# Kernel tuning notes

Measured on AMD Instinct MI355X. Metric: run time of the kernel, lower is better.

Reference implementation:

```python
import jax, jax.numpy as jnp
import numpy as np

N = 50000      # nodes
E = 800000     # edges (avg degree 16)
G = 256        # graphs in batch
IN = 128       # in_channels
H = 256        # hidden_channels
L = 4          # num_layers


def setup_inputs() -> dict:
    key = jax.random.key(0)
    ks = jax.random.split(key, 16)
    x = jax.random.normal(ks[0], (N, IN), dtype=jnp.float32)
    edge_index = jax.random.randint(ks[1], (2, E), 0, N, dtype=jnp.int64)
    batch = jnp.sort(jax.random.randint(ks[2], (N,), 0, G, dtype=jnp.int64))
    s_in = 1.0 / np.sqrt(IN)
    s_h = 1.0 / np.sqrt(H)
    return {
        "x": x,
        "edge_index": edge_index,
        "batch": batch,
        "w1_0": jax.random.normal(ks[3], (IN, H), jnp.float32) * s_in,
        "b1_0": jnp.zeros((H,), jnp.float32),
        "w2_0": jax.random.normal(ks[4], (H, H), jnp.float32) * s_h,
        "b2_0": jnp.zeros((H,), jnp.float32),
        "w1s": jax.random.normal(ks[5], (L - 1, H, H), jnp.float32) * s_h,
        "b1s": jnp.zeros((L - 1, H), jnp.float32),
        "w2s": jax.random.normal(ks[6], (L - 1, H, H), jnp.float32) * s_h,
        "b2s": jnp.zeros((L - 1, H), jnp.float32),
    }


def reference(x, edge_index, batch, w1_0, b1_0, w2_0, b2_0, w1s, b1s, w2s, b2s):
    n_nodes = x.shape[0]
    src, dst = edge_index[0], edge_index[1]

    def gin_layer(h, w1, b1, w2, b2):
        # scatter-add neighbor aggregation: out[i] = sum_{(j->i)} h[j]
        agg = jax.ops.segment_sum(h[src], dst, num_segments=n_nodes)
        z = h + agg  # GIN with eps = 0: (1+eps)*x + aggr
        z = jax.nn.relu(z @ w1 + b1) @ w2 + b2  # MLP: Linear-ReLU-Linear
        return jax.nn.relu(z)  # outer F.relu in forward

    h = gin_layer(x, w1_0, b1_0, w2_0, b2_0)
    for i in range(L - 1):  # small fixed layer loop
        h = gin_layer(h, w1s[i], b1s[i], w2s[i], b2s[i])

    # global_add_pool: per-graph segment sum -> [G, H]
    return jax.ops.segment_sum(h, batch, num_segments=G)
```

## Files before the change

kernel.cpp:

```cpp
#include <hip/hip_runtime.h>
#include <hip/hip_bf16.h>

#define NN 50000
#define NE 800000
#define NG 256
#define CIN 128
#define CH 256

typedef unsigned short u16;
typedef unsigned int u32;
typedef __attribute__((ext_vector_type(8))) short short8;
typedef __attribute__((ext_vector_type(8))) unsigned short ushort8;
typedef __attribute__((ext_vector_type(4))) float f32x4;

__device__ __forceinline__ float bf2f(u16 u) { return __uint_as_float(((u32)u) << 16); }
__device__ __forceinline__ u16 f2bf(float f) {
    u32 u = __float_as_uint(f);
    return (u16)((u + 0x7fffu + ((u >> 16) & 1u)) >> 16);
}

__global__ void k_prep(const float* __restrict__ x, u16* __restrict__ xb,
                       const float* __restrict__ w1_0, const float* __restrict__ w2_0,
                       const float* __restrict__ w1s, const float* __restrict__ w2s,
                       u16* __restrict__ Wp, int* __restrict__ deg_fill,
                       int* __restrict__ gs, int* __restrict__ ge,
                       float* __restrict__ outf) {
    int t = blockIdx.x * 256 + threadIdx.x;
    if (t < 2 * NN) deg_fill[t] = 0;
    if (t < NG) { gs[t] = 0; ge[t] = 0; }
    if (t < NG * CH) outf[t] = 0.f;
    if (t < NN * CIN / 4) {
        float4 v = ((const float4*)x)[t];
        ushort4 o; o.x = f2bf(v.x); o.y = f2bf(v.y); o.z = f2bf(v.z); o.w = f2bf(v.w);
        ((ushort4*)xb)[t] = o;
    }
    if (t < CIN * CH + 7 * CH * CH) {
        const float* Wsrc; int rem;
        if (t < CIN * CH) { Wsrc = w1_0; rem = t; }
        else {
            int o = t - CIN * CH;
            int m = o >> 16; rem = o & 65535;
            Wsrc = (m == 0) ? w2_0
                 : (m <= 3) ? w1s + (size_t)(m - 1) * 65536
                            : w2s + (size_t)(m - 4) * 65536;
        }
        int j = rem & 7, lane = (rem >> 3) & 63, nt = (rem >> 9) & 15, kb = rem >> 13;
        int k = kb * 32 + ((lane >> 4) << 3) + j;
        int nc = nt * 16 + (lane & 15);
        Wp[t] = f2bf(Wsrc[k * CH + nc]);
    }
}

__global__ void k_count_deg_bounds(const int* __restrict__ dst, int* __restrict__ deg,
                                   const int* __restrict__ batch,
                                   int* __restrict__ gs, int* __restrict__ ge) {
    int e = blockIdx.x * 256 + threadIdx.x;
    if (e < NE) atomicAdd(&deg[dst[e]], 1);
    if (e < NN) {
        int b = batch[e];
        if (e == 0 || batch[e - 1] != b) gs[b] = e;
        if (e == NN - 1 || batch[e + 1] != b) ge[b] = e + 1;
    }
}

__global__ void k_scan1(const int* __restrict__ deg, int* __restrict__ bsum) {
    __shared__ int sd[256];
    int base = blockIdx.x * 1024, t = threadIdx.x, s = 0;
    for (int j = 0; j < 4; j++) { int i = base + t * 4 + j; if (i < NN) s += deg[i]; }
    sd[t] = s; __syncthreads();
    for (int off = 128; off > 0; off >>= 1) { if (t < off) sd[t] += sd[t + off]; __syncthreads(); }
    if (t == 0) bsum[blockIdx.x] = sd[0];
}

__global__ void k_scan2(int* bsum, int nb, int* row_ptr) {
    int lane = threadIdx.x;
    int v = (lane < nb) ? bsum[lane] : 0;
    int s = v;
    for (int off = 1; off < 64; off <<= 1) {
        int t = __shfl_up(s, off, 64);
        if (lane >= off) s += t;
    }
    if (lane < nb) bsum[lane] = s - v;
    if (lane == 0) row_ptr[NN] = NE;
}

__global__ void k_scan3(const int* __restrict__ deg, const int* __restrict__ bsum,
                        int* __restrict__ row_ptr) {
    __shared__ int sd[256];
    int base = blockIdx.x * 1024, t = threadIdx.x;
    int v[4]; int s = 0;
    for (int j = 0; j < 4; j++) { int i = base + t * 4 + j; v[j] = (i < NN) ? deg[i] : 0; s += v[j]; }
    sd[t] = s; __syncthreads();
    for (int off = 1; off < 256; off <<= 1) {
        int tmp = (t >= off) ? sd[t - off] : 0; __syncthreads();
        sd[t] += tmp; __syncthreads();
    }
    int run = bsum[blockIdx.x] + sd[t] - s;
    for (int j = 0; j < 4; j++) { int i = base + t * 4 + j; if (i < NN) row_ptr[i] = run; run += v[j]; }
}

__global__ void k_fill(const int* __restrict__ src, const int* __restrict__ dst,
                       const int* __restrict__ row_ptr, int* __restrict__ fill,
                       int* __restrict__ col) {
    int e = blockIdx.x * 256 + threadIdx.x;
    if (e < NE) {
        int d = dst[e];
        int pos = row_ptr[d] + atomicAdd(&fill[d], 1);
        col[pos] = src[e];
    }
}

#define ZS 264
template <int K1>
__global__ __launch_bounds__(256, 8) void k_layer(const u16* __restrict__ G,
                                                  const int* __restrict__ row_ptr,
                                                  const int* __restrict__ col,
                                                  const u16* __restrict__ Wp1,
                                                  const float* __restrict__ b1,
                                                  const u16* __restrict__ Wp2,
                                                  const float* __restrict__ b2,
                                                  u16* __restrict__ out) {
    __shared__ __align__(16) u16 zs[32 * ZS];
    const int tid = threadIdx.x;
    const int wave = tid >> 6, lane = tid & 63;
    const int quad = lane >> 4, l16 = lane & 15;
    const int m0 = blockIdx.x * 32;

    constexpr int LPR = K1 / 8;
    constexpr int RPG = 64 / LPR;
    const int sub = lane / LPR;
    const int c0 = (lane % LPR) * 8;
    for (int g = 0; g < 8; g += RPG) {
        int lr = wave * 8 + g + sub;
        int r = m0 + lr; if (r >= NN) r = NN - 1;
        const u16* base = G + c0;
        float a[8];
        ushort8 sv = *(const ushort8*)(base + (size_t)r * K1);
#pragma unroll
        for (int i = 0; i < 8; i++) a[i] = bf2f(sv[i]);
        int beg = row_ptr[r], end = row_ptr[r + 1];
        int e = beg;
        for (; e + 4 <= end; e += 4) {
            ushort8 v0 = *(const ushort8*)(base + (size_t)col[e] * K1);
            ushort8 v1 = *(const ushort8*)(base + (size_t)col[e + 1] * K1);
            ushort8 v2 = *(const ushort8*)(base + (size_t)col[e + 2] * K1);
            ushort8 v3 = *(const ushort8*)(base + (size_t)col[e + 3] * K1);
#pragma unroll
            for (int i = 0; i < 8; i++)
                a[i] += bf2f(v0[i]) + bf2f(v1[i]) + bf2f(v2[i]) + bf2f(v3[i]);
        }
        for (; e < end; e++) {
            ushort8 nv = *(const ushort8*)(base + (size_t)col[e] * K1);
#pragma unroll
            for (int i = 0; i < 8; i++) a[i] += bf2f(nv[i]);
        }
        ushort8 o;
#pragma unroll
        for (int i = 0; i < 8; i++) o[i] = f2bf(a[i]);
        *(ushort8*)(zs + lr * ZS + c0) = o;
    }
    __syncthreads();

    f32x4 acc[2][4];
#pragma unroll
    for (int ri = 0; ri < 2; ri++)
#pragma unroll
        for (int nj = 0; nj < 4; nj++) acc[ri][nj] = (f32x4){0.f, 0.f, 0.f, 0.f};

    const u16* w1b = Wp1 + (wave * 4) * 512 + lane * 8;
    const u16* w2b = Wp2 + (wave * 4) * 512 + lane * 8;
    constexpr int KB1 = K1 / 32;
    short8 b_cur[4], b_nxt[4];
#pragma unroll
    for (int nj = 0; nj < 4; nj++) b_cur[nj] = *(const short8*)(w1b + nj * 512);

#pragma unroll
    for (int kb = 0; kb < KB1; kb++) {
        int kn = (kb + 1 < KB1) ? (kb + 1) : kb;
#pragma unroll
        for (int nj = 0; nj < 4; nj++)
            b_nxt[nj] = *(const short8*)(w1b + kn * 8192 + nj * 512);
        short8 a[2];
#pragma unroll
        for (int ri = 0; ri < 2; ri++)
            a[ri] = *(const short8*)(zs + (ri * 16 + l16) * ZS + kb * 32 + quad * 8);
#pragma unroll
        for (int nj = 0; nj < 4; nj++)
#pragma unroll
            for (int ri = 0; ri < 2; ri++)
                acc[ri][nj] = __builtin_amdgcn_mfma_f32_16x16x32_bf16(a[ri], b_cur[nj], acc[ri][nj], 0, 0, 0);
#pragma unroll
        for (int nj = 0; nj < 4; nj++) b_cur[nj] = b_nxt[nj];
    }

    short8 b2_cur[4];
#pragma unroll
    for (int nj = 0; nj < 4; nj++) b2_cur[nj] = *(const short8*)(w2b + nj * 512);

    __syncthreads();

#pragma unroll
    for (int nj = 0; nj < 4; nj++) {
        int cc = wave * 64 + nj * 16 + l16;
        float bv = b1[cc];
#pragma unroll
        for (int ri = 0; ri < 2; ri++) {
            f32x4 v = acc[ri][nj];
#pragma unroll
            for (int j = 0; j < 4; j++)
                zs[(ri * 16 + quad * 4 + j) * ZS + cc] = f2bf(fmaxf(v[j] + bv, 0.f));
        }
    }
    __syncthreads();

#pragma unroll
    for (int ri = 0; ri < 2; ri++)
#pragma unroll
        for (int nj = 0; nj < 4; nj++) acc[ri][nj] = (f32x4){0.f, 0.f, 0.f, 0.f};

#pragma unroll
    for (int kb = 0; kb < 8; kb++) {
        int kn = (kb + 1 < 8) ? (kb + 1) : kb;
#pragma unroll
        for (int nj = 0; nj < 4; nj++)
            b_nxt[nj] = *(const short8*)(w2b + kn * 8192 + nj * 512);
        short8 a[2];
#pragma unroll
        for (int ri = 0; ri < 2; ri++)
            a[ri] = *(const short8*)(zs + (ri * 16 + l16) * ZS + kb * 32 + quad * 8);
#pragma unroll
        for (int nj = 0; nj < 4; nj++)
#pragma unroll
            for (int ri = 0; ri < 2; ri++)
                acc[ri][nj] = __builtin_amdgcn_mfma_f32_16x16x32_bf16(a[ri], b2_cur[nj], acc[ri][nj], 0, 0, 0);
#pragma unroll
        for (int nj = 0; nj < 4; nj++) b2_cur[nj] = b_nxt[nj];
    }
    __syncthreads();

#pragma unroll
    for (int nj = 0; nj < 4; nj++) {
        int cc = wave * 64 + nj * 16 + l16;
        float bv = b2[cc];
#pragma unroll
        for (int ri = 0; ri < 2; ri++) {
            f32x4 v = acc[ri][nj];
#pragma unroll
            for (int j = 0; j < 4; j++)
                zs[(ri * 16 + quad * 4 + j) * ZS + cc] = f2bf(fmaxf(v[j] + bv, 0.f));
        }
    }
    __syncthreads();

    int row = tid >> 3, cb = (tid & 7) * 32;
    if (m0 + row < NN) {
        uint4* dst = (uint4*)(out + (size_t)(m0 + row) * CH + cb);
        const u16* srcp = zs + row * ZS + cb;
#pragma unroll
        for (int c = 0; c < 4; c++) dst[c] = *(const uint4*)(srcp + c * 8);
    }
}

__global__ void k_pool(const u16* __restrict__ h, const int* __restrict__ gs,
                       const int* __restrict__ ge, float* __restrict__ out) {
    int g = blockIdx.x >> 2, part = blockIdx.x & 3, c = threadIdx.x;
    int s = gs[g], e = ge[g];
    float acc = 0.f;
    for (int i = s + part; i < e; i += 4) acc += bf2f(h[(size_t)i * CH + c]);
    atomicAdd(&out[g * CH + c], acc);
}

extern "C" void kernel_launch(void* const* d_in, const int* in_sizes, int n_in,
                              void* d_out, int out_size, void* d_ws, size_t ws_size,
                              hipStream_t stream) {
    const float* x     = (const float*)d_in[0];
    const int*   ei    = (const int*)d_in[1];
    const int*   batch = (const int*)d_in[2];
    const float* w1_0  = (const float*)d_in[3];
    const float* b1_0  = (const float*)d_in[4];
    const float* w2_0  = (const float*)d_in[5];
    const float* b2_0  = (const float*)d_in[6];
    const float* w1s   = (const float*)d_in[7];
    const float* b1s   = (const float*)d_in[8];
    const float* w2s   = (const float*)d_in[9];
    const float* b2s   = (const float*)d_in[10];
    float* out = (float*)d_out;

    char* p = (char*)d_ws;
    u16* Hb  = (u16*)p; p += (size_t)NN * CH * 2;
    u16* Tb  = (u16*)p; p += (size_t)NN * CH * 2;
    u16* xb  = (u16*)p; p += (size_t)NN * CIN * 2;
    u16* WpA = (u16*)p; p += (size_t)(CIN * CH + 7 * CH * CH) * 2;
    int* row_ptr = (int*)p; p += (size_t)(NN + 1) * 4;
    int* deg  = (int*)p; p += (size_t)NN * 4;
    int* fill = (int*)p; p += (size_t)NN * 4;
    int* col  = (int*)p; p += (size_t)NE * 4;
    int* bsum = (int*)p; p += 256 * 4;
    int* gs   = (int*)p; p += NG * 4;
    int* ge   = (int*)p; p += NG * 4;

    u16* Wp1_0 = WpA;
    u16* Wp2_0 = Wp1_0 + CIN * CH;
    u16* Wp1sA = Wp2_0 + CH * CH;
    u16* Wp2sA = Wp1sA + 3 * CH * CH;

    const int* srcv = ei;
    const int* dstv = ei + NE;

    int nb = (NN + 1023) / 1024;

    hipLaunchKernelGGL(k_prep, dim3((NN * CIN / 4 + 255) / 256), dim3(256), 0, stream,
                       x, xb, w1_0, w2_0, w1s, w2s, WpA, deg, gs, ge, out);

    hipLaunchKernelGGL(k_count_deg_bounds, dim3((NE + 255) / 256), dim3(256), 0, stream,
                       dstv, deg, batch, gs, ge);
    hipLaunchKernelGGL(k_scan1, dim3(nb), dim3(256), 0, stream, deg, bsum);
    hipLaunchKernelGGL(k_scan2, dim3(1), dim3(64), 0, stream, bsum, nb, row_ptr);
    hipLaunchKernelGGL(k_scan3, dim3(nb), dim3(256), 0, stream, deg, bsum, row_ptr);
    hipLaunchKernelGGL(k_fill, dim3((NE + 255) / 256), dim3(256), 0, stream, srcv, dstv, row_ptr, fill, col);

    int layerBlocks = (NN + 31) / 32;

    hipLaunchKernelGGL((k_layer<128>), dim3(layerBlocks), dim3(256), 0, stream,
                       xb, row_ptr, col, Wp1_0, b1_0, Wp2_0, b2_0, Hb);
    hipLaunchKernelGGL((k_layer<256>), dim3(layerBlocks), dim3(256), 0, stream,
                       Hb, row_ptr, col, Wp1sA, b1s, Wp2sA, b2s, Tb);
    hipLaunchKernelGGL((k_layer<256>), dim3(layerBlocks), dim3(256), 0, stream,
                       Tb, row_ptr, col, Wp1sA + (size_t)CH * CH, b1s + CH,
                       Wp2sA + (size_t)CH * CH, b2s + CH, Hb);
    hipLaunchKernelGGL((k_layer<256>), dim3(layerBlocks), dim3(256), 0, stream,
                       Hb, row_ptr, col, Wp1sA + (size_t)2 * CH * CH, b1s + 2 * CH,
                       Wp2sA + (size_t)2 * CH * CH, b2s + 2 * CH, Tb);

    hipLaunchKernelGGL(k_pool, dim3(NG * 4), dim3(256), 0, stream, Tb, gs, ge, out);
}
```

Measured before the change: 484.7 us.

## Fuse global add pool into last GIN layer and widen gather unroll

The final layer kernel now accumulates its ReLU output per graph directly from shared memory, using the sorted batch vector, and issues atomicAdds into the pooled output. This removes the last layer's full hidden-state write, the separate pool kernel and the graph-boundary computation. The neighbor gather loop is also unrolled to eight outstanding loads instead of four to raise memory-level parallelism. The cost is more atomics on the output (one per block segment per channel) and higher register pressure in the gather loop.

```diff
diff --git a/kernel.cpp b/kernel.cpp
--- a/kernel.cpp
+++ b/kernel.cpp
@@ -23,11 +23,9 @@
                        const float* __restrict__ w1_0, const float* __restrict__ w2_0,
                        const float* __restrict__ w1s, const float* __restrict__ w2s,
                        u16* __restrict__ Wp, int* __restrict__ deg_fill,
-                       int* __restrict__ gs, int* __restrict__ ge,
                        float* __restrict__ outf) {
     int t = blockIdx.x * 256 + threadIdx.x;
     if (t < 2 * NN) deg_fill[t] = 0;
-    if (t < NG) { gs[t] = 0; ge[t] = 0; }
     if (t < NG * CH) outf[t] = 0.f;
     if (t < NN * CIN / 4) {
         float4 v = ((const float4*)x)[t];
@@ -51,16 +49,9 @@
     }
 }
 
-__global__ void k_count_deg_bounds(const int* __restrict__ dst, int* __restrict__ deg,
-                                   const int* __restrict__ batch,
-                                   int* __restrict__ gs, int* __restrict__ ge) {
+__global__ void k_count_deg(const int* __restrict__ dst, int* __restrict__ deg) {
     int e = blockIdx.x * 256 + threadIdx.x;
     if (e < NE) atomicAdd(&deg[dst[e]], 1);
-    if (e < NN) {
-        int b = batch[e];
-        if (e == 0 || batch[e - 1] != b) gs[b] = e;
-        if (e == NN - 1 || batch[e + 1] != b) ge[b] = e + 1;
-    }
 }
 
 __global__ void k_scan1(const int* __restrict__ deg, int* __restrict__ bsum) {
@@ -111,7 +102,7 @@
 }
 
 #define ZS 264
-template <int K1>
+template <int K1, bool POOL>
 __global__ __launch_bounds__(256, 8) void k_layer(const u16* __restrict__ G,
                                                   const int* __restrict__ row_ptr,
                                                   const int* __restrict__ col,
@@ -119,7 +110,9 @@
                                                   const float* __restrict__ b1,
                                                   const u16* __restrict__ Wp2,
                                                   const float* __restrict__ b2,
-                                                  u16* __restrict__ out) {
+                                                  u16* __restrict__ out,
+                                                  const int* __restrict__ batchp,
+                                                  float* __restrict__ outf) {
     __shared__ __align__(16) u16 zs[32 * ZS];
     const int tid = threadIdx.x;
     const int wave = tid >> 6, lane = tid & 63;
@@ -140,14 +133,15 @@
         for (int i = 0; i < 8; i++) a[i] = bf2f(sv[i]);
         int beg = row_ptr[r], end = row_ptr[r + 1];
         int e = beg;
-        for (; e + 4 <= end; e += 4) {
-            ushort8 v0 = *(const ushort8*)(base + (size_t)col[e] * K1);
-            ushort8 v1 = *(const ushort8*)(base + (size_t)col[e + 1] * K1);
-            ushort8 v2 = *(const ushort8*)(base + (size_t)col[e + 2] * K1);
-            ushort8 v3 = *(const ushort8*)(base + (size_t)col[e + 3] * K1);
-#pragma unroll
-            for (int i = 0; i < 8; i++)
-                a[i] += bf2f(v0[i]) + bf2f(v1[i]) + bf2f(v2[i]) + bf2f(v3[i]);
+        for (; e + 8 <= end; e += 8) {
+            ushort8 v[8];
+#pragma unroll
+            for (int q = 0; q < 8; q++)
+                v[q] = *(const ushort8*)(base + (size_t)col[e + q] * K1);
+#pragma unroll
+            for (int q = 0; q < 8; q++)
+#pragma unroll
+                for (int i = 0; i < 8; i++) a[i] += bf2f(v[q][i]);
         }
         for (; e < end; e++) {
             ushort8 nv = *(const ushort8*)(base + (size_t)col[e] * K1);
@@ -252,22 +246,30 @@
     }
     __syncthreads();
 
-    int row = tid >> 3, cb = (tid & 7) * 32;
-    if (m0 + row < NN) {
-        uint4* dst = (uint4*)(out + (size_t)(m0 + row) * CH + cb);
-        const u16* srcp = zs + row * ZS + cb;
-#pragma unroll
-        for (int c = 0; c < 4; c++) dst[c] = *(const uint4*)(srcp + c * 8);
-    }
-}
-
-__global__ void k_pool(const u16* __restrict__ h, const int* __restrict__ gs,
-                       const int* __restrict__ ge, float* __restrict__ out) {
-    int g = blockIdx.x >> 2, part = blockIdx.x & 3, c = threadIdx.x;
-    int s = gs[g], e = ge[g];
-    float acc = 0.f;
-    for (int i = s + part; i < e; i += 4) acc += bf2f(h[(size_t)i * CH + c]);
-    atomicAdd(&out[g * CH + c], acc);
+    if (!POOL) {
+        int row = tid >> 3, cb = (tid & 7) * 32;
+        if (m0 + row < NN) {
+            uint4* dst = (uint4*)(out + (size_t)(m0 + row) * CH + cb);
+            const u16* srcp = zs + row * ZS + cb;
+#pragma unroll
+            for (int c = 0; c < 4; c++) dst[c] = *(const uint4*)(srcp + c * 8);
+        }
+    } else {
+        int c = tid;
+        float acc2 = 0.f;
+        int cur_g = batchp[m0];
+        for (int row = 0; row < 32; row++) {
+            int r = m0 + row;
+            if (r >= NN) break;
+            int g = batchp[r];
+            if (g != cur_g) {
+                atomicAdd(&outf[cur_g * CH + c], acc2);
+                acc2 = 0.f; cur_g = g;
+            }
+            acc2 += bf2f(zs[row * ZS + c]);
+        }
+        atomicAdd(&outf[cur_g * CH + c], acc2);
+    }
 }
 
 extern "C" void kernel_launch(void* const* d_in, const int* in_sizes, int n_in,
@@ -296,8 +298,6 @@
     int* fill = (int*)p; p += (size_t)NN * 4;
     int* col  = (int*)p; p += (size_t)NE * 4;
     int* bsum = (int*)p; p += 256 * 4;
-    int* gs   = (int*)p; p += NG * 4;
-    int* ge   = (int*)p; p += NG * 4;
 
     u16* Wp1_0 = WpA;
     u16* Wp2_0 = Wp1_0 + CIN * CH;
@@ -310,10 +310,9 @@
     int nb = (NN + 1023) / 1024;
 
     hipLaunchKernelGGL(k_prep, dim3((NN * CIN / 4 + 255) / 256), dim3(256), 0, stream,
-                       x, xb, w1_0, w2_0, w1s, w2s, WpA, deg, gs, ge, out);
-
-    hipLaunchKernelGGL(k_count_deg_bounds, dim3((NE + 255) / 256), dim3(256), 0, stream,
-                       dstv, deg, batch, gs, ge);
+                       x, xb, w1_0, w2_0, w1s, w2s, WpA, deg, out);
+
+    hipLaunchKernelGGL(k_count_deg, dim3((NE + 255) / 256), dim3(256), 0, stream, dstv, deg);
     hipLaunchKernelGGL(k_scan1, dim3(nb), dim3(256), 0, stream, deg, bsum);
     hipLaunchKernelGGL(k_scan2, dim3(1), dim3(64), 0, stream, bsum, nb, row_ptr);
     hipLaunchKernelGGL(k_scan3, dim3(nb), dim3(256), 0, stream, deg, bsum, row_ptr);
@@ -321,16 +320,14 @@
 
     int layerBlocks = (NN + 31) / 32;
 
-    hipLaunchKernelGGL((k_layer<128>), dim3(layerBlocks), dim3(256), 0, stream,
-                       xb, row_ptr, col, Wp1_0, b1_0, Wp2_0, b2_0, Hb);
-    hipLaunchKernelGGL((k_layer<256>), dim3(layerBlocks), dim3(256), 0, stream,
-                       Hb, row_ptr, col, Wp1sA, b1s, Wp2sA, b2s, Tb);
-    hipLaunchKernelGGL((k_layer<256>), dim3(layerBlocks), dim3(256), 0, stream,
+    hipLaunchKernelGGL((k_layer<128, false>), dim3(layerBlocks), dim3(256), 0, stream,
+                       xb, row_ptr, col, Wp1_0, b1_0, Wp2_0, b2_0, Hb, batch, out);
+    hipLaunchKernelGGL((k_layer<256, false>), dim3(layerBlocks), dim3(256), 0, stream,
+                       Hb, row_ptr, col, Wp1sA, b1s, Wp2sA, b2s, Tb, batch, out);
+    hipLaunchKernelGGL((k_layer<256, false>), dim3(layerBlocks), dim3(256), 0, stream,
                        Tb, row_ptr, col, Wp1sA + (size_t)CH * CH, b1s + CH,
-                       Wp2sA + (size_t)CH * CH, b2s + CH, Hb);
-    hipLaunchKernelGGL((k_layer<256>), dim3(layerBlocks), dim3(256), 0, stream,
+                       Wp2sA + (size_t)CH * CH, b2s + CH, Hb, batch, out);
+    hipLaunchKernelGGL((k_layer<256, true>), dim3(layerBlocks), dim3(256), 0, stream,
                        Hb, row_ptr, col, Wp1sA + (size_t)2 * CH * CH, b1s + 2 * CH,
-                       Wp2sA + (size_t)2 * CH * CH, b2s + 2 * CH, Tb);
-
-    hipLaunchKernelGGL(k_pool, dim3(NG * 4), dim3(256), 0, stream, Tb, gs, ge, out);
-}
+                       Wp2sA + (size_t)2 * CH * CH, b2s + 2 * CH, (u16*)nullptr, batch, out);
+}
```

Result: faster. 463.7 us (-4.3%).
